# Optimization experiments

Hardware: AMD Instinct MI355X
Metric: run time of the kernel (lower is better)

## Reference

```python
import jax, jax.numpy as jnp
import numpy as np

N, E = 50000, 800000
IN_DIM, HIDDEN, OUT_DIM, LAYERS = 128, 64, 40, 3


def setup_inputs() -> dict:
    key = jax.random.key(0)
    ks = jax.random.split(key, 12)
    glorot = lambda k, fi, fo: jax.random.normal(k, (fi, fo), jnp.float32) * np.sqrt(2.0 / (fi + fo)).astype(np.float32)
    return {
        "x": jax.random.normal(ks[0], (N, IN_DIM), jnp.float32),
        "edge_index": jax.random.randint(ks[1], (2, E), 0, N, jnp.int64),
        "edge_weight": jax.random.uniform(ks[2], (E,), jnp.float32),
        "W1": glorot(ks[3], IN_DIM, HIDDEN), "b1": jnp.zeros((HIDDEN,), jnp.float32),
        "W2": glorot(ks[4], HIDDEN, HIDDEN), "b2": jnp.zeros((HIDDEN,), jnp.float32),
        "W3": glorot(ks[5], HIDDEN, HIDDEN), "b3": jnp.zeros((HIDDEN,), jnp.float32),
        "Wlin": glorot(ks[6], HIDDEN * LAYERS, OUT_DIM), "blin": jnp.zeros((OUT_DIM,), jnp.float32),
    }


def reference(x, edge_index, edge_weight, W1, b1, W2, b2, W3, b3, Wlin, blin):
    src, dst = edge_index[0], edge_index[1]

    def gcn_conv(h, W, b):
        # GCNConv with normalize=False: linear transform, then weighted sum aggregation at dst, then bias.
        h = h @ W                                   # [N, hidden]
        msg = h[src] * edge_weight[:, None]          # [E, hidden] gather + scale
        agg = jax.ops.segment_sum(msg, dst, num_segments=h.shape[0])  # scatter-add
        return agg + b

    outs = []
    h = x
    for W, b in ((W1, b1), (W2, b2), (W3, b3)):
        h = jax.nn.relu(gcn_conv(h, W, b))           # dropout is identity at inference
        outs.append(h)

    hjk = jnp.concatenate(outs, axis=-1)             # JumpingKnowledge mode='cat' -> [N, hidden*layers]
    return hjk @ Wlin + blin                         # [N, out_dim]
```

## Files before the change

### kernel.cpp

```cpp
#include <hip/hip_runtime.h>

#define HID 64
#define JK_DIM 192
#define OUT_DIM 40
#define AP 136
#define HP 72
#define AP2 200

typedef __attribute__((ext_vector_type(8))) short bf16x8;
typedef __attribute__((ext_vector_type(4))) float f32x4;

__device__ inline unsigned short f2b(float f) {
    unsigned u = __float_as_uint(f);
    unsigned r = u + 0x7FFF + ((u >> 16) & 1);
    return (unsigned short)(r >> 16);
}
__device__ inline float b2f(unsigned short u) {
    return __uint_as_float(((unsigned)u) << 16);
}
__device__ inline float blo(unsigned u) { return __uint_as_float(u << 16); }
__device__ inline float bhi(unsigned u) { return __uint_as_float(u & 0xFFFF0000u); }
__device__ inline unsigned pack2(float a, float b) {
    return (unsigned)f2b(a) | ((unsigned)f2b(b) << 16);
}

__global__ __launch_bounds__(256) void prep(int* __restrict__ deg, int n,
                                            int* __restrict__ gctr) {
    int i = blockIdx.x * 256 + threadIdx.x;
    if (i == 0) gctr[0] = 0;
    if (i < n) deg[i] = 0;
}

__global__ __launch_bounds__(256) void hist_dst(const int* __restrict__ dst,
                                                int* __restrict__ deg,
                                                unsigned short* __restrict__ rank,
                                                int E, int part) {
    int p = blockIdx.x & 7;
    int bid = blockIdx.x >> 3;
    int nblk = gridDim.x >> 3;
    int lo = p * part, hi = lo + part;
    int E4 = E >> 2;
    for (int q = bid * 256 + threadIdx.x; q < E4; q += nblk * 256) {
        int4 d4 = ((const int4*)dst)[q];
        int e = q * 4;
        if (d4.x >= lo && d4.x < hi) rank[e + 0] = (unsigned short)atomicAdd(&deg[d4.x], 1);
        if (d4.y >= lo && d4.y < hi) rank[e + 1] = (unsigned short)atomicAdd(&deg[d4.y], 1);
        if (d4.z >= lo && d4.z < hi) rank[e + 2] = (unsigned short)atomicAdd(&deg[d4.z], 1);
        if (d4.w >= lo && d4.w < hi) rank[e + 3] = (unsigned short)atomicAdd(&deg[d4.w], 1);
    }
    if (bid == 0 && threadIdx.x < (E & 3)) {
        int e = (E & ~3) + threadIdx.x;
        int d = dst[e];
        if (d >= lo && d < hi) rank[e] = (unsigned short)atomicAdd(&deg[d], 1);
    }
}

__global__ __launch_bounds__(256) void scan_fused(const int* __restrict__ deg,
                                                  int* __restrict__ off,
                                                  int* __restrict__ gctr, int n) {
    __shared__ int tmp[256];
    __shared__ int base;
    int i = blockIdx.x * 256 + threadIdx.x;
    int v = (i < n) ? deg[i] : 0;
    tmp[threadIdx.x] = v;
    __syncthreads();
    for (int d = 1; d < 256; d <<= 1) {
        int t = (threadIdx.x >= d) ? tmp[threadIdx.x - d] : 0;
        __syncthreads();
        tmp[threadIdx.x] += t;
        __syncthreads();
    }
    if (threadIdx.x == 255) base = atomicAdd(gctr, tmp[255]);
    __syncthreads();
    if (i < n) off[i] = base + tmp[threadIdx.x] - v;
}

__global__ __launch_bounds__(256) void fill_and_gemm(
        const int* __restrict__ src, const int* __restrict__ dst,
        const float* __restrict__ ew, const int* __restrict__ off,
        const unsigned short* __restrict__ rank,
        unsigned* __restrict__ ecsr, int E,
        const float* __restrict__ x, const float* __restrict__ W1,
        unsigned short* __restrict__ linb, int n, int nFill) {
    __shared__ unsigned short Ah[64 * AP];
    __shared__ unsigned short Wt[64 * AP];
    int tid = threadIdx.x;
    if ((int)blockIdx.x < nFill) {
        int q = blockIdx.x * 256 + tid;
        int E4 = E >> 2;
        if (q < E4) {
            int4 d4 = ((const int4*)dst)[q];
            int4 s4 = ((const int4*)src)[q];
            float4 wv = ((const float4*)ew)[q];
            ushort4 r4 = ((const ushort4*)rank)[q];
            ecsr[off[d4.x] + r4.x] = (unsigned)s4.x | ((unsigned)f2b(wv.x) << 16);
            ecsr[off[d4.y] + r4.y] = (unsigned)s4.y | ((unsigned)f2b(wv.y) << 16);
            ecsr[off[d4.z] + r4.z] = (unsigned)s4.z | ((unsigned)f2b(wv.z) << 16);
            ecsr[off[d4.w] + r4.w] = (unsigned)s4.w | ((unsigned)f2b(wv.w) << 16);
        }
        if (blockIdx.x == 0 && tid < (E & 3)) {
            int e = (E & ~3) + tid;
            int d = dst[e];
            ecsr[off[d] + rank[e]] = (unsigned)src[e] | ((unsigned)f2b(ew[e]) << 16);
        }
        return;
    }
    int row0 = (blockIdx.x - nFill) * 64;
    if (row0 >= n) return;
    for (int i = tid; i < 64 * 32; i += 256) {
        int r = i >> 5;
        int c4 = (i & 31) * 4;
        int grow = row0 + r;
        if (grow >= n) grow = n - 1;
        float4 v = *(const float4*)(x + (long)grow * 128 + c4);
        ushort4 o;
        o.x = f2b(v.x); o.y = f2b(v.y); o.z = f2b(v.z); o.w = f2b(v.w);
        *(ushort4*)(Ah + r * AP + c4) = o;
    }
    for (int i = tid; i < 128 * 16; i += 256) {
        int k = i >> 4;
        int n4 = (i & 15) * 4;
        float4 v = *(const float4*)(W1 + (long)k * 64 + n4);
        Wt[(n4 + 0) * AP + k] = f2b(v.x);
        Wt[(n4 + 1) * AP + k] = f2b(v.y);
        Wt[(n4 + 2) * AP + k] = f2b(v.z);
        Wt[(n4 + 3) * AP + k] = f2b(v.w);
    }
    __syncthreads();

    int wave = tid >> 6;
    int lane = tid & 63;
    int lr = lane & 15;
    int lk = (lane >> 4) * 8;
    f32x4 acc[4];
#pragma unroll
    for (int nf = 0; nf < 4; ++nf) acc[nf] = (f32x4){0.f, 0.f, 0.f, 0.f};
#pragma unroll
    for (int k0 = 0; k0 < 128; k0 += 32) {
        bf16x8 a = *(const bf16x8*)(Ah + (wave * 16 + lr) * AP + k0 + lk);
#pragma unroll
        for (int nf = 0; nf < 4; ++nf) {
            bf16x8 b = *(const bf16x8*)(Wt + (nf * 16 + lr) * AP + k0 + lk);
            acc[nf] = __builtin_amdgcn_mfma_f32_16x16x32_bf16(a, b, acc[nf], 0, 0, 0);
        }
    }
    int mbase = wave * 16 + (lane >> 4) * 4;
#pragma unroll
    for (int nf = 0; nf < 4; ++nf) {
#pragma unroll
        for (int r = 0; r < 4; ++r) {
            int grow = row0 + mbase + r;
            if (grow < n)
                linb[(long)grow * HID + nf * 16 + lr] = f2b(acc[nf][r]);
        }
    }
}

__global__ __launch_bounds__(256) void aggregate(const unsigned short* __restrict__ linb,
                                                 const unsigned* __restrict__ ecsr,
                                                 const int* __restrict__ off,
                                                 const int* __restrict__ deg,
                                                 const float* __restrict__ bias,
                                                 unsigned short* __restrict__ hout, int n) {
    int cl = threadIdx.x & 7;
    float4 bLo = *(const float4*)(bias + cl * 8);
    float4 bHi = *(const float4*)(bias + cl * 8 + 4);
    int grp = (blockIdx.x * 256 + threadIdx.x) >> 3;
    int ngrp = (gridDim.x * 256) >> 3;
    for (int node = grp; node < n; node += ngrp) {
        int start = off[node];
        int cnt = deg[node];
        float acc[8];
#pragma unroll
        for (int i = 0; i < 8; ++i) acc[i] = 0.f;

        int s[8];
        float w[8];
#pragma unroll
        for (int t = 0; t < 8; ++t) {
            s[t] = 0; w[t] = 0.f;
            if (t < cnt) {
                unsigned m = ecsr[start + t];
                s[t] = (int)(m & 0xFFFFu);
                w[t] = b2f((unsigned short)(m >> 16));
            }
        }
        for (int bb = 0; bb < cnt; bb += 8) {
            int s2[8];
            float w2[8];
#pragma unroll
            for (int t = 0; t < 8; ++t) {
                int e = bb + 8 + t;
                s2[t] = 0; w2[t] = 0.f;
                if (e < cnt) {
                    unsigned m = ecsr[start + e];
                    s2[t] = (int)(m & 0xFFFFu);
                    w2[t] = b2f((unsigned short)(m >> 16));
                }
            }
            uint4 u[8];
#pragma unroll
            for (int t = 0; t < 8; ++t)
                u[t] = *(const uint4*)(linb + (long)s[t] * HID + cl * 8);
#pragma unroll
            for (int t = 0; t < 8; ++t) {
                acc[0] += blo(u[t].x) * w[t];
                acc[1] += bhi(u[t].x) * w[t];
                acc[2] += blo(u[t].y) * w[t];
                acc[3] += bhi(u[t].y) * w[t];
                acc[4] += blo(u[t].z) * w[t];
                acc[5] += bhi(u[t].z) * w[t];
                acc[6] += blo(u[t].w) * w[t];
                acc[7] += bhi(u[t].w) * w[t];
            }
#pragma unroll
            for (int t = 0; t < 8; ++t) { s[t] = s2[t]; w[t] = w2[t]; }
        }

        uint4 o;
        o.x = pack2(fmaxf(acc[0] + bLo.x, 0.f), fmaxf(acc[1] + bLo.y, 0.f));
        o.y = pack2(fmaxf(acc[2] + bLo.z, 0.f), fmaxf(acc[3] + bLo.w, 0.f));
        o.z = pack2(fmaxf(acc[4] + bHi.x, 0.f), fmaxf(acc[5] + bHi.y, 0.f));
        o.w = pack2(fmaxf(acc[6] + bHi.z, 0.f), fmaxf(acc[7] + bHi.w, 0.f));
        *(uint4*)(hout + (long)node * JK_DIM + cl * 8) = o;
    }
}

__global__ __launch_bounds__(256) void agg_transform(
        const unsigned short* __restrict__ hprev,
        const unsigned* __restrict__ ecsr,
        const int* __restrict__ off, const int* __restrict__ deg,
        const float* __restrict__ W, const float* __restrict__ bias,
        unsigned short* __restrict__ hout, int n) {
    __shared__ unsigned short Hs[64 * HP];
    __shared__ unsigned short Wt[64 * HP];
    int tid = threadIdx.x;
    int row0 = blockIdx.x * 64;
    if (row0 >= n) return;
    for (int i = tid; i < 64 * 16; i += 256) {
        int k = i >> 4;
        int n4 = (i & 15) * 4;
        float4 v = *(const float4*)(W + (long)k * 64 + n4);
        Wt[(n4 + 0) * HP + k] = f2b(v.x);
        Wt[(n4 + 1) * HP + k] = f2b(v.y);
        Wt[(n4 + 2) * HP + k] = f2b(v.z);
        Wt[(n4 + 3) * HP + k] = f2b(v.w);
    }
    int cl = tid & 7;
    int g0 = tid >> 3;
    for (int gi = 0; gi < 2; ++gi) {
        int lrow = g0 + gi * 32;
        int node = row0 + lrow;
        float acc[8];
#pragma unroll
        for (int i = 0; i < 8; ++i) acc[i] = 0.f;
        if (node < n) {
            int start = off[node];
            int cnt = deg[node];
            int s[8];
            float w[8];
#pragma unroll
            for (int t = 0; t < 8; ++t) {
                s[t] = 0; w[t] = 0.f;
                if (t < cnt) {
                    unsigned m = ecsr[start + t];
                    s[t] = (int)(m & 0xFFFFu);
                    w[t] = b2f((unsigned short)(m >> 16));
                }
            }
            for (int bb = 0; bb < cnt; bb += 8) {
                int s2[8];
                float w2[8];
#pragma unroll
                for (int t = 0; t < 8; ++t) {
                    int e = bb + 8 + t;
                    s2[t] = 0; w2[t] = 0.f;
                    if (e < cnt) {
                        unsigned m = ecsr[start + e];
                        s2[t] = (int)(m & 0xFFFFu);
                        w2[t] = b2f((unsigned short)(m >> 16));
                    }
                }
                uint4 u[8];
#pragma unroll
                for (int t = 0; t < 8; ++t)
                    u[t] = *(const uint4*)(hprev + (long)s[t] * JK_DIM + cl * 8);
#pragma unroll
                for (int t = 0; t < 8; ++t) {
                    acc[0] += blo(u[t].x) * w[t];
                    acc[1] += bhi(u[t].x) * w[t];
                    acc[2] += blo(u[t].y) * w[t];
                    acc[3] += bhi(u[t].y) * w[t];
                    acc[4] += blo(u[t].z) * w[t];
                    acc[5] += bhi(u[t].z) * w[t];
                    acc[6] += blo(u[t].w) * w[t];
                    acc[7] += bhi(u[t].w) * w[t];
                }
#pragma unroll
                for (int t = 0; t < 8; ++t) { s[t] = s2[t]; w[t] = w2[t]; }
            }
        }
        uint4 o;
        o.x = pack2(acc[0], acc[1]);
        o.y = pack2(acc[2], acc[3]);
        o.z = pack2(acc[4], acc[5]);
        o.w = pack2(acc[6], acc[7]);
        *(uint4*)(Hs + lrow * HP + cl * 8) = o;
    }
    __syncthreads();
    int wave = tid >> 6;
    int lane = tid & 63;
    int lr = lane & 15;
    int lk = (lane >> 4) * 8;
    f32x4 d[4];
#pragma unroll
    for (int nf = 0; nf < 4; ++nf) d[nf] = (f32x4){0.f, 0.f, 0.f, 0.f};
#pragma unroll
    for (int k0 = 0; k0 < 64; k0 += 32) {
        bf16x8 a = *(const bf16x8*)(Hs + (wave * 16 + lr) * HP + k0 + lk);
#pragma unroll
        for (int nf = 0; nf < 4; ++nf) {
            bf16x8 b = *(const bf16x8*)(Wt + (nf * 16 + lr) * HP + k0 + lk);
            d[nf] = __builtin_amdgcn_mfma_f32_16x16x32_bf16(a, b, d[nf], 0, 0, 0);
        }
    }
    int mbase = wave * 16 + (lane >> 4) * 4;
#pragma unroll
    for (int nf = 0; nf < 4; ++nf) {
        float bv = bias[nf * 16 + lr];
#pragma unroll
        for (int r = 0; r < 4; ++r) {
            int grow = row0 + mbase + r;
            if (grow < n)
                hout[(long)grow * JK_DIM + nf * 16 + lr] = f2b(fmaxf(d[nf][r] + bv, 0.f));
        }
    }
}

__global__ __launch_bounds__(256) void jk_final(
        const unsigned short* __restrict__ hprev,
        const unsigned* __restrict__ ecsr,
        const int* __restrict__ off, const int* __restrict__ deg,
        const float* __restrict__ W, const float* __restrict__ bias,
        const unsigned short* __restrict__ hcat,
        const float* __restrict__ Wlin,
        const float* __restrict__ blin,
        float* __restrict__ outp, int n) {
    __shared__ unsigned short pool[112 * AP2];
    unsigned short* Hs = pool;
    unsigned short* Wt = pool + 64 * HP;
    int tid = threadIdx.x;
    int row0 = blockIdx.x * 64;
    if (row0 >= n) return;
    for (int i = tid; i < 64 * 16; i += 256) {
        int k = i >> 4;
        int n4 = (i & 15) * 4;
        float4 v = *(const float4*)(W + (long)k * 64 + n4);
        Wt[(n4 + 0) * HP + k] = f2b(v.x);
        Wt[(n4 + 1) * HP + k] = f2b(v.y);
        Wt[(n4 + 2) * HP + k] = f2b(v.z);
        Wt[(n4 + 3) * HP + k] = f2b(v.w);
    }
    int cl = tid & 7;
    int g0 = tid >> 3;
    for (int gi = 0; gi < 2; ++gi) {
        int lrow = g0 + gi * 32;
        int node = row0 + lrow;
        float acc[8];
#pragma unroll
        for (int i = 0; i < 8; ++i) acc[i] = 0.f;
        if (node < n) {
            int start = off[node];
            int cnt = deg[node];
            int s[8];
            float w[8];
#pragma unroll
            for (int t = 0; t < 8; ++t) {
                s[t] = 0; w[t] = 0.f;
                if (t < cnt) {
                    unsigned m = ecsr[start + t];
                    s[t] = (int)(m & 0xFFFFu);
                    w[t] = b2f((unsigned short)(m >> 16));
                }
            }
            for (int bb = 0; bb < cnt; bb += 8) {
                int s2[8];
                float w2[8];
#pragma unroll
                for (int t = 0; t < 8; ++t) {
                    int e = bb + 8 + t;
                    s2[t] = 0; w2[t] = 0.f;
                    if (e < cnt) {
                        unsigned m = ecsr[start + e];
                        s2[t] = (int)(m & 0xFFFFu);
                        w2[t] = b2f((unsigned short)(m >> 16));
                    }
                }
                uint4 u[8];
#pragma unroll
                for (int t = 0; t < 8; ++t)
                    u[t] = *(const uint4*)(hprev + (long)s[t] * JK_DIM + cl * 8);
#pragma unroll
                for (int t = 0; t < 8; ++t) {
                    acc[0] += blo(u[t].x) * w[t];
                    acc[1] += bhi(u[t].x) * w[t];
                    acc[2] += blo(u[t].y) * w[t];
                    acc[3] += bhi(u[t].y) * w[t];
                    acc[4] += blo(u[t].z) * w[t];
                    acc[5] += bhi(u[t].z) * w[t];
                    acc[6] += blo(u[t].w) * w[t];
                    acc[7] += bhi(u[t].w) * w[t];
                }
#pragma unroll
                for (int t = 0; t < 8; ++t) { s[t] = s2[t]; w[t] = w2[t]; }
            }
        }
        uint4 o;
        o.x = pack2(acc[0], acc[1]);
        o.y = pack2(acc[2], acc[3]);
        o.z = pack2(acc[4], acc[5]);
        o.w = pack2(acc[6], acc[7]);
        *(uint4*)(Hs + lrow * HP + cl * 8) = o;
    }
    __syncthreads();
    int wave = tid >> 6;
    int lane = tid & 63;
    int lr = lane & 15;
    int lk = (lane >> 4) * 8;
    f32x4 d[4];
#pragma unroll
    for (int nf = 0; nf < 4; ++nf) d[nf] = (f32x4){0.f, 0.f, 0.f, 0.f};
#pragma unroll
    for (int k0 = 0; k0 < 64; k0 += 32) {
        bf16x8 a = *(const bf16x8*)(Hs + (wave * 16 + lr) * HP + k0 + lk);
#pragma unroll
        for (int nf = 0; nf < 4; ++nf) {
            bf16x8 b = *(const bf16x8*)(Wt + (nf * 16 + lr) * HP + k0 + lk);
            d[nf] = __builtin_amdgcn_mfma_f32_16x16x32_bf16(a, b, d[nf], 0, 0, 0);
        }
    }
    __syncthreads();
    unsigned short* Acat = pool;
    unsigned short* WtL  = pool + 64 * AP2;
    for (int i = tid; i < 64 * 16; i += 256) {
        int r = i >> 4;
        int q8 = (i & 15) * 8;
        int grow = row0 + r;
        if (grow >= n) grow = n - 1;
        *(uint4*)(Acat + r * AP2 + q8) = *(const uint4*)(hcat + (long)grow * JK_DIM + q8);
    }
    for (int i = tid; i < JK_DIM * OUT_DIM; i += 256) {
        int k = i / OUT_DIM;
        int c = i - k * OUT_DIM;
        WtL[c * AP2 + k] = f2b(Wlin[i]);
    }
    for (int i = tid; i < 8 * JK_DIM; i += 256) {
        int c = 40 + i / JK_DIM;
        int k = i - (i / JK_DIM) * JK_DIM;
        WtL[c * AP2 + k] = 0;
    }
    int mbase = wave * 16 + (lane >> 4) * 4;
#pragma unroll
    for (int nf = 0; nf < 4; ++nf) {
        float bv = bias[nf * 16 + lr];
#pragma unroll
        for (int r = 0; r < 4; ++r)
            Acat[(mbase + r) * AP2 + 128 + nf * 16 + lr] = f2b(fmaxf(d[nf][r] + bv, 0.f));
    }
    __syncthreads();
    f32x4 acc2[3];
#pragma unroll
    for (int nf = 0; nf < 3; ++nf) acc2[nf] = (f32x4){0.f, 0.f, 0.f, 0.f};
#pragma unroll
    for (int k0 = 0; k0 < 192; k0 += 32) {
        bf16x8 a = *(const bf16x8*)(Acat + (wave * 16 + lr) * AP2 + k0 + lk);
#pragma unroll
        for (int nf = 0; nf < 3; ++nf) {
            bf16x8 b = *(const bf16x8*)(WtL + (nf * 16 + lr) * AP2 + k0 + lk);
            acc2[nf] = __builtin_amdgcn_mfma_f32_16x16x32_bf16(a, b, acc2[nf], 0, 0, 0);
        }
    }
#pragma unroll
    for (int nf = 0; nf < 3; ++nf) {
        int col = nf * 16 + lr;
        if (col < OUT_DIM) {
            float bb = blin[col];
#pragma unroll
            for (int r = 0; r < 4; ++r) {
                int grow = row0 + mbase + r;
                if (grow < n)
                    outp[(long)grow * OUT_DIM + col] = acc2[nf][r] + bb;
            }
        }
    }
}

extern "C" void kernel_launch(void* const* d_in, const int* in_sizes, int n_in,
                              void* d_out, int out_size, void* d_ws, size_t ws_size,
                              hipStream_t stream) {
    const float* x    = (const float*)d_in[0];
    const int*   ei   = (const int*)d_in[1];
    const float* ew   = (const float*)d_in[2];
    const float* W1   = (const float*)d_in[3];
    const float* b1   = (const float*)d_in[4];
    const float* W2   = (const float*)d_in[5];
    const float* b2   = (const float*)d_in[6];
    const float* W3   = (const float*)d_in[7];
    const float* b3   = (const float*)d_in[8];
    const float* Wlin = (const float*)d_in[9];
    const float* blin = (const float*)d_in[10];
    float* out = (float*)d_out;

    const int N = in_sizes[0] / 128;
    const int E = in_sizes[2];
    const int* src = ei;
    const int* dst = ei + E;
    const int PART = (N + 7) / 8;

    char* wsb = (char*)d_ws;
    unsigned short* linb  = (unsigned short*)wsb;   wsb += (long)N * HID * 2;
    unsigned short* hcatb = (unsigned short*)wsb;   wsb += (long)N * JK_DIM * 2;
    int* deg    = (int*)wsb;                        wsb += (long)N * 4;
    int* off    = (int*)wsb;                        wsb += (long)N * 4;
    int* bsum   = (int*)wsb;                        wsb += 256 * 4;
    unsigned* ecsr = (unsigned*)wsb;
    unsigned short* rank = hcatb;
    int* gctr = bsum;

    dim3 blk(256);
    const int nblkN = (N + 255) / 256;
    dim3 gN(nblkN);
    dim3 gHist(8 * 104);
    const int nFill = ((E >> 2) + 255) / 256;
    const int nGemm = (N + 63) / 64;
    dim3 gFG(nFill + nGemm);
    dim3 gTile((N + 63) / 64);
    dim3 gAgg((N + 31) / 32);

    unsigned short* h1 = hcatb;
    unsigned short* h2 = hcatb + HID;

    prep<<<gN, blk, 0, stream>>>(deg, N, gctr);
    hist_dst<<<gHist, blk, 0, stream>>>(dst, deg, rank, E, PART);
    scan_fused<<<gN, blk, 0, stream>>>(deg, off, gctr, N);

    fill_and_gemm<<<gFG, blk, 0, stream>>>(src, dst, ew, off, rank, ecsr, E,
                                           x, W1, linb, N, nFill);
    aggregate<<<gAgg, blk, 0, stream>>>(linb, ecsr, off, deg, b1, h1, N);

    agg_transform<<<gTile, blk, 0, stream>>>(h1, ecsr, off, deg, W2, b2, h2, N);

    jk_final<<<gTile, blk, 0, stream>>>(h2, ecsr, off, deg, W3, b3,
                                        hcatb, Wlin, blin, out, N);
}
```

Baseline: 245.3 us.

## Pre-transpose weights to bf16 once and chunk JK final GEMM through smaller LDS

Weight matrices are now converted to bf16 and transposed once in the prep kernel, so the GEMM kernels load them with vectorized 16-byte copies instead of each block doing scalar transposed LDS stores with conversion. The JK final linear layer is split into three 64-wide K chunks that reuse the existing Hs/Wt LDS buffers. This shrinks shared memory from 112x200 to 128x72 shorts, which should allow higher occupancy. The cost is extra syncthreads between chunks and a little more global traffic for the chunked hcat loads.

```diff
diff --git a/kernel.cpp b/kernel.cpp
--- a/kernel.cpp
+++ b/kernel.cpp
@@ -5,7 +5,6 @@
 #define OUT_DIM 40
 #define AP 136
 #define HP 72
-#define AP2 200
 
 typedef __attribute__((ext_vector_type(8))) short bf16x8;
 typedef __attribute__((ext_vector_type(4))) float f32x4;
@@ -25,10 +24,31 @@
 }
 
 __global__ __launch_bounds__(256) void prep(int* __restrict__ deg, int n,
-                                            int* __restrict__ gctr) {
+                                            int* __restrict__ gctr,
+                                            const float* __restrict__ W1,
+                                            const float* __restrict__ W2,
+                                            const float* __restrict__ W3,
+                                            const float* __restrict__ Wlin,
+                                            unsigned short* __restrict__ W1T,
+                                            unsigned short* __restrict__ W2T,
+                                            unsigned short* __restrict__ W3T,
+                                            unsigned short* __restrict__ WlinT) {
     int i = blockIdx.x * 256 + threadIdx.x;
     if (i == 0) gctr[0] = 0;
     if (i < n) deg[i] = 0;
+    if (i < 64 * 128) {
+        int nn = i >> 7, k = i & 127;
+        W1T[i] = f2b(W1[k * 64 + nn]);
+    }
+    if (i < 64 * 64) {
+        int nn = i >> 6, k = i & 63;
+        W2T[i] = f2b(W2[k * 64 + nn]);
+        W3T[i] = f2b(W3[k * 64 + nn]);
+    }
+    if (i < 48 * JK_DIM) {
+        int c = i / JK_DIM, k = i - c * JK_DIM;
+        WlinT[i] = (c < OUT_DIM) ? f2b(Wlin[k * OUT_DIM + c]) : (unsigned short)0;
+    }
 }
 
 __global__ __launch_bounds__(256) void hist_dst(const int* __restrict__ dst,
@@ -80,7 +100,7 @@
         const float* __restrict__ ew, const int* __restrict__ off,
         const unsigned short* __restrict__ rank,
         unsigned* __restrict__ ecsr, int E,
-        const float* __restrict__ x, const float* __restrict__ W1,
+        const float* __restrict__ x, const unsigned short* __restrict__ W1T,
         unsigned short* __restrict__ linb, int n, int nFill) {
     __shared__ unsigned short Ah[64 * AP];
     __shared__ unsigned short Wt[64 * AP];
@@ -117,14 +137,10 @@
         o.x = f2b(v.x); o.y = f2b(v.y); o.z = f2b(v.z); o.w = f2b(v.w);
         *(ushort4*)(Ah + r * AP + c4) = o;
     }
-    for (int i = tid; i < 128 * 16; i += 256) {
-        int k = i >> 4;
-        int n4 = (i & 15) * 4;
-        float4 v = *(const float4*)(W1 + (long)k * 64 + n4);
-        Wt[(n4 + 0) * AP + k] = f2b(v.x);
-        Wt[(n4 + 1) * AP + k] = f2b(v.y);
-        Wt[(n4 + 2) * AP + k] = f2b(v.z);
-        Wt[(n4 + 3) * AP + k] = f2b(v.w);
+    for (int i = tid; i < 64 * 16; i += 256) {
+        int nn = i >> 4;
+        int k8 = (i & 15) * 8;
+        *(uint4*)(Wt + nn * AP + k8) = *(const uint4*)(W1T + nn * 128 + k8);
     }
     __syncthreads();
 
@@ -230,21 +246,17 @@
         const unsigned short* __restrict__ hprev,
         const unsigned* __restrict__ ecsr,
         const int* __restrict__ off, const int* __restrict__ deg,
-        const float* __restrict__ W, const float* __restrict__ bias,
+        const unsigned short* __restrict__ WT, const float* __restrict__ bias,
         unsigned short* __restrict__ hout, int n) {
     __shared__ unsigned short Hs[64 * HP];
     __shared__ unsigned short Wt[64 * HP];
     int tid = threadIdx.x;
     int row0 = blockIdx.x * 64;
     if (row0 >= n) return;
-    for (int i = tid; i < 64 * 16; i += 256) {
-        int k = i >> 4;
-        int n4 = (i & 15) * 4;
-        float4 v = *(const float4*)(W + (long)k * 64 + n4);
-        Wt[(n4 + 0) * HP + k] = f2b(v.x);
-        Wt[(n4 + 1) * HP + k] = f2b(v.y);
-        Wt[(n4 + 2) * HP + k] = f2b(v.z);
-        Wt[(n4 + 3) * HP + k] = f2b(v.w);
+    for (int i = tid; i < 64 * 8; i += 256) {
+        int nn = i >> 3;
+        int k8 = (i & 7) * 8;
+        *(uint4*)(Wt + nn * HP + k8) = *(const uint4*)(WT + nn * 64 + k8);
     }
     int cl = tid & 7;
     int g0 = tid >> 3;
@@ -341,25 +353,21 @@
         const unsigned short* __restrict__ hprev,
         const unsigned* __restrict__ ecsr,
         const int* __restrict__ off, const int* __restrict__ deg,
-        const float* __restrict__ W, const float* __restrict__ bias,
+        const unsigned short* __restrict__ W3T, const float* __restrict__ bias,
         const unsigned short* __restrict__ hcat,
-        const float* __restrict__ Wlin,
+        const unsigned short* __restrict__ WlinT,
         const float* __restrict__ blin,
         float* __restrict__ outp, int n) {
-    __shared__ unsigned short pool[112 * AP2];
+    __shared__ unsigned short pool[128 * HP];
     unsigned short* Hs = pool;
     unsigned short* Wt = pool + 64 * HP;
     int tid = threadIdx.x;
     int row0 = blockIdx.x * 64;
     if (row0 >= n) return;
-    for (int i = tid; i < 64 * 16; i += 256) {
-        int k = i >> 4;
-        int n4 = (i & 15) * 4;
-        float4 v = *(const float4*)(W + (long)k * 64 + n4);
-        Wt[(n4 + 0) * HP + k] = f2b(v.x);
-        Wt[(n4 + 1) * HP + k] = f2b(v.y);
-        Wt[(n4 + 2) * HP + k] = f2b(v.z);
-        Wt[(n4 + 3) * HP + k] = f2b(v.w);
+    for (int i = tid; i < 64 * 8; i += 256) {
+        int nn = i >> 3;
+        int k8 = (i & 7) * 8;
+        *(uint4*)(Wt + nn * HP + k8) = *(const uint4*)(W3T + nn * 64 + k8);
     }
     int cl = tid & 7;
     int g0 = tid >> 3;
@@ -439,44 +447,58 @@
             d[nf] = __builtin_amdgcn_mfma_f32_16x16x32_bf16(a, b, d[nf], 0, 0, 0);
         }
     }
-    __syncthreads();
-    unsigned short* Acat = pool;
-    unsigned short* WtL  = pool + 64 * AP2;
-    for (int i = tid; i < 64 * 16; i += 256) {
-        int r = i >> 4;
-        int q8 = (i & 15) * 8;
-        int grow = row0 + r;
-        if (grow >= n) grow = n - 1;
-        *(uint4*)(Acat + r * AP2 + q8) = *(const uint4*)(hcat + (long)grow * JK_DIM + q8);
-    }
-    for (int i = tid; i < JK_DIM * OUT_DIM; i += 256) {
-        int k = i / OUT_DIM;
-        int c = i - k * OUT_DIM;
-        WtL[c * AP2 + k] = f2b(Wlin[i]);
-    }
-    for (int i = tid; i < 8 * JK_DIM; i += 256) {
-        int c = 40 + i / JK_DIM;
-        int k = i - (i / JK_DIM) * JK_DIM;
-        WtL[c * AP2 + k] = 0;
-    }
     int mbase = wave * 16 + (lane >> 4) * 4;
+    unsigned short* As = Hs;
+    unsigned short* WL = Wt;
+    f32x4 acc2[3];
+#pragma unroll
+    for (int nf = 0; nf < 3; ++nf) acc2[nf] = (f32x4){0.f, 0.f, 0.f, 0.f};
+    for (int ch = 0; ch < 2; ++ch) {
+        int cb = ch * 64;
+        __syncthreads();
+        for (int i = tid; i < 64 * 8; i += 256) {
+            int r = i >> 3;
+            int q8 = (i & 7) * 8;
+            int grow = row0 + r;
+            if (grow >= n) grow = n - 1;
+            *(uint4*)(As + r * HP + q8) = *(const uint4*)(hcat + (long)grow * JK_DIM + cb + q8);
+        }
+        for (int i = tid; i < 48 * 8; i += 256) {
+            int c = i >> 3;
+            int k8 = (i & 7) * 8;
+            *(uint4*)(WL + c * HP + k8) = *(const uint4*)(WlinT + c * JK_DIM + cb + k8);
+        }
+        __syncthreads();
+#pragma unroll
+        for (int k0 = 0; k0 < 64; k0 += 32) {
+            bf16x8 a = *(const bf16x8*)(As + (wave * 16 + lr) * HP + k0 + lk);
+#pragma unroll
+            for (int nf = 0; nf < 3; ++nf) {
+                bf16x8 b = *(const bf16x8*)(WL + (nf * 16 + lr) * HP + k0 + lk);
+                acc2[nf] = __builtin_amdgcn_mfma_f32_16x16x32_bf16(a, b, acc2[nf], 0, 0, 0);
+            }
+        }
+    }
+    __syncthreads();
 #pragma unroll
     for (int nf = 0; nf < 4; ++nf) {
         float bv = bias[nf * 16 + lr];
 #pragma unroll
         for (int r = 0; r < 4; ++r)
-            Acat[(mbase + r) * AP2 + 128 + nf * 16 + lr] = f2b(fmaxf(d[nf][r] + bv, 0.f));
-    }
-    __syncthreads();
-    f32x4 acc2[3];
-#pragma unroll
-    for (int nf = 0; nf < 3; ++nf) acc2[nf] = (f32x4){0.f, 0.f, 0.f, 0.f};
-#pragma unroll
-    for (int k0 = 0; k0 < 192; k0 += 32) {
-        bf16x8 a = *(const bf16x8*)(Acat + (wave * 16 + lr) * AP2 + k0 + lk);
+            As[(mbase + r) * HP + nf * 16 + lr] = f2b(fmaxf(d[nf][r] + bv, 0.f));
+    }
+    for (int i = tid; i < 48 * 8; i += 256) {
+        int c = i >> 3;
+        int k8 = (i & 7) * 8;
+        *(uint4*)(WL + c * HP + k8) = *(const uint4*)(WlinT + c * JK_DIM + 128 + k8);
+    }
+    __syncthreads();
+#pragma unroll
+    for (int k0 = 0; k0 < 64; k0 += 32) {
+        bf16x8 a = *(const bf16x8*)(As + (wave * 16 + lr) * HP + k0 + lk);
 #pragma unroll
         for (int nf = 0; nf < 3; ++nf) {
-            bf16x8 b = *(const bf16x8*)(WtL + (nf * 16 + lr) * AP2 + k0 + lk);
+            bf16x8 b = *(const bf16x8*)(WL + (nf * 16 + lr) * HP + k0 + lk);
             acc2[nf] = __builtin_amdgcn_mfma_f32_16x16x32_bf16(a, b, acc2[nf], 0, 0, 0);
         }
     }
@@ -523,6 +545,10 @@
     int* deg    = (int*)wsb;                        wsb += (long)N * 4;
     int* off    = (int*)wsb;                        wsb += (long)N * 4;
     int* bsum   = (int*)wsb;                        wsb += 256 * 4;
+    unsigned short* W1T  = (unsigned short*)wsb;    wsb += 64 * 128 * 2;
+    unsigned short* W2T  = (unsigned short*)wsb;    wsb += 64 * 64 * 2;
+    unsigned short* W3T  = (unsigned short*)wsb;    wsb += 64 * 64 * 2;
+    unsigned short* WlinT = (unsigned short*)wsb;   wsb += 48 * JK_DIM * 2;
     unsigned* ecsr = (unsigned*)wsb;
     unsigned short* rank = hcatb;
     int* gctr = bsum;
@@ -540,16 +566,17 @@
     unsigned short* h1 = hcatb;
     unsigned short* h2 = hcatb + HID;
 
-    prep<<<gN, blk, 0, stream>>>(deg, N, gctr);
+    prep<<<gN, blk, 0, stream>>>(deg, N, gctr, W1, W2, W3, Wlin,
+                                 W1T, W2T, W3T, WlinT);
     hist_dst<<<gHist, blk, 0, stream>>>(dst, deg, rank, E, PART);
     scan_fused<<<gN, blk, 0, stream>>>(deg, off, gctr, N);
 
     fill_and_gemm<<<gFG, blk, 0, stream>>>(src, dst, ew, off, rank, ecsr, E,
-                                           x, W1, linb, N, nFill);
+                                           x, W1T, linb, N, nFill);
     aggregate<<<gAgg, blk, 0, stream>>>(linb, ecsr, off, deg, b1, h1, N);
 
-    agg_transform<<<gTile, blk, 0, stream>>>(h1, ecsr, off, deg, W2, b2, h2, N);
-
-    jk_final<<<gTile, blk, 0, stream>>>(h2, ecsr, off, deg, W3, b3,
-                                        hcatb, Wlin, blin, out, N);
-}
+    agg_transform<<<gTile, blk, 0, stream>>>(h1, ecsr, off, deg, W2T, b2, h2, N);
+
+    jk_final<<<gTile, blk, 0, stream>>>(h2, ecsr, off, deg, W3T, b3,
+                                        hcatb, WlinT, blin, out, N);
+}
```

Measured after the change: 233.7 us. 4.7% less time.
